# Kernel tuning notes

Measured on AMD Instinct MI355X. Metric: run time of the kernel, lower is better.

## Reference

```python
import jax, jax.numpy as jnp
import numpy as np

B, S, E, H, V = 64, 400, 512, 512, 32000


def setup_inputs() -> dict:
    key = jax.random.key(0)
    ks = jax.random.split(key, 16)
    sc = lambda fan: 1.0 / np.sqrt(fan)
    u = lambda k, shape, fan: jax.random.uniform(k, shape, jnp.float32, -sc(fan), sc(fan))
    mask = jax.random.randint(ks[3], (B, S), 0, 2).astype(bool)
    mask = mask.at[:, 0].set(True)  # ensure at least one valid position per row
    return {
        "decoder_input": jax.random.normal(ks[0], (B, E), jnp.float32),
        "previous_hidden_state": jax.random.normal(ks[1], (B, H), jnp.float32),
        "encoder_output": jax.random.normal(ks[2], (B, S, 2 * H), jnp.float32),
        "mask": mask,
        # GRUCell params (torch layout: weight_ih [3H,E], weight_hh [3H,H])
        "w_ih": u(ks[4], (3 * H, E), H),
        "w_hh": u(ks[5], (3 * H, H), H),
        "b_ih": u(ks[6], (3 * H,), H),
        "b_hh": u(ks[7], (3 * H,), H),
        # Attention params
        "Wh_w": u(ks[8], (H, 2 * H), 2 * H),
        "Wh_b": u(ks[9], (H,), 2 * H),
        "Ws_w": u(ks[10], (H, H), H),
        "Ws_b": u(ks[11], (H,), H),
        "vatt_w": u(ks[12], (1, H), H),  # Linear(H,1,bias=False)
        # Output projections
        "V_w": u(ks[13], (H, 3 * H), 3 * H),
        "V_b": u(ks[13], (H,), 3 * H),
        "Vhat_w": u(ks[14], (V, H), H),
        "Vhat_b": u(ks[15], (V,), H),
    }


def reference(decoder_input, previous_hidden_state, encoder_output, mask,
              w_ih, w_hh, b_ih, b_hh, Wh_w, Wh_b, Ws_w, Ws_b, vatt_w,
              V_w, V_b, Vhat_w, Vhat_b):
    # --- GRUCell step (torch semantics) ---
    gi = decoder_input @ w_ih.T + b_ih                  # [B, 3H]
    gh = previous_hidden_state @ w_hh.T + b_hh          # [B, 3H]
    i_r, i_z, i_n = jnp.split(gi, 3, axis=-1)
    h_r, h_z, h_n = jnp.split(gh, 3, axis=-1)
    r = jax.nn.sigmoid(i_r + h_r)
    z = jax.nn.sigmoid(i_z + h_z)
    n = jnp.tanh(i_n + r * h_n)
    hidden = (1.0 - z) * n + z * previous_hidden_state  # [B, H]

    # --- Additive (Bahdanau) attention ---
    feat = jnp.tanh(encoder_output @ Wh_w.T + Wh_b
                    + (hidden @ Ws_w.T + Ws_b)[:, None, :])   # [B, S, H]
    scores = jnp.einsum('bsh,h->bs', feat, vatt_w[0])          # [B, S]
    scores = jnp.where(mask, scores, -jnp.inf)
    attn_dist = jax.nn.softmax(scores, axis=-1)                # [B, S]

    # --- Context + output projection ---
    context_vector = jnp.einsum('bs,bsd->bd', attn_dist, encoder_output)  # [B, 2H]
    out = jnp.concatenate([hidden, context_vector], axis=-1) @ V_w.T + V_b  # [B, H]
    logits = out @ Vhat_w.T + Vhat_b                                        # [B, V]
    vocab_dist = jax.nn.softmax(logits, axis=-1)
    return (vocab_dist, attn_dist, context_vector, hidden)
```

## Files before the change

### kernel.cpp

```cpp
#include <hip/hip_runtime.h>
#include <hip/hip_bf16.h>
#include <stdint.h>

#define DI __device__ __forceinline__

using f32x4 = __attribute__((ext_vector_type(4))) float;
using s16x8 = __attribute__((ext_vector_type(8))) short;

#define BB 64
#define SS 400
#define HH 512
#define VVOC 32000
#define MTOT (BB*SS)

DI short bf16r(float f){
  __hip_bfloat16 h = __float2bfloat16(f);
  union { __hip_bfloat16 h; short s; } u; u.h = h; return u.s;
}
DI float sigm(float x){ return 1.f/(1.f + __expf(-x)); }
DI float tanhfast(float x){ x = fminf(x, 12.f); float e = __expf(2.f*x); return (e-1.f)/(e+1.f); }

DI void gload16b(const __hip_bfloat16* g, short* l){
  __builtin_amdgcn_global_load_lds(
      (const __attribute__((address_space(1))) __hip_bfloat16*)g,
      (__attribute__((address_space(3))) short*)l, 16, 0, 0);
}

DI float blkmax(float v, float* red, int t){
  #pragma unroll
  for (int o = 32; o; o >>= 1) v = fmaxf(v, __shfl_xor(v, o));
  if ((t & 63) == 0) red[t >> 6] = v;
  __syncthreads();
  v = fmaxf(fmaxf(red[0], red[1]), fmaxf(red[2], red[3]));
  __syncthreads();
  return v;
}
DI float blksum(float v, float* red, int t){
  #pragma unroll
  for (int o = 32; o; o >>= 1) v += __shfl_xor(v, o);
  if ((t & 63) == 0) red[t >> 6] = v;
  __syncthreads();
  v = red[0] + red[1] + red[2] + red[3];
  __syncthreads();
  return v;
}

DI s16x8 cvt8v(f32x4 a, f32x4 b){
  s16x8 o;
  o[0]=bf16r(a[0]); o[1]=bf16r(a[1]); o[2]=bf16r(a[2]); o[3]=bf16r(a[3]);
  o[4]=bf16r(b[0]); o[5]=bf16r(b[1]); o[6]=bf16r(b[2]); o[7]=bf16r(b[3]);
  return o;
}
DI s16x8 cvt8(const float* src){
  return cvt8v(((const f32x4*)src)[0], ((const f32x4*)src)[1]);
}

DI s16x8 fragload16(const short* tile, int rbase, int kk, int l){
  int r = rbase + (l & 15);
  int c = (kk >> 3) + (l >> 4);
  int slot = c ^ (r & 7);
  return *(const s16x8*)(tile + r*64 + slot*8);
}

DI void mfma_small_body(const float* __restrict__ A, const float* __restrict__ W,
                        float* __restrict__ P, int K, int N, int c0, int kseg,
                        short* lsa, short* lsb, int t)
{
  const int kbeg = kseg*64;
  const int l = t & 63, w = t >> 6;
  #pragma unroll
  for (int q = 0; q < 2; ++q) {
    int it = q*256 + t;
    int r = it >> 3, c = it & 7;
    int slot = (c ^ (r & 7)) << 3;
    *(s16x8*)(lsa + r*64 + slot) = cvt8(A + (size_t)r*K + kbeg + c*8);
    *(s16x8*)(lsb + r*64 + slot) = cvt8(W + (size_t)(c0 + r)*K + kbeg + c*8);
  }
  __syncthreads();
  f32x4 acc[4];
  #pragma unroll
  for (int m = 0; m < 4; ++m) { f32x4 z = {0.f,0.f,0.f,0.f}; acc[m] = z; }
  #pragma unroll
  for (int kk = 0; kk < 64; kk += 32) {
    s16x8 bf = fragload16(lsb, w*16, kk, l);
    #pragma unroll
    for (int m = 0; m < 4; ++m) {
      s16x8 af = fragload16(lsa, m*16, kk, l);
      acc[m] = __builtin_amdgcn_mfma_f32_16x16x32_bf16(af, bf, acc[m], 0, 0, 0);
    }
  }
  const int kq = l >> 4, lc = l & 15;
  const int col = c0 + w*16 + lc;
  size_t pbase = (size_t)kseg * 64 * N;
  #pragma unroll
  for (int m = 0; m < 4; ++m)
    #pragma unroll
    for (int j = 0; j < 4; ++j)
      P[pbase + (size_t)(m*16 + kq*4 + j)*N + col] = acc[m][j];
}

__global__ __launch_bounds__(256) void k_pre(
    const float* __restrict__ enc, const float* __restrict__ wh,
    short* __restrict__ enc16, short* __restrict__ wh16,
    const unsigned int* __restrict__ mask, int mwords, int* __restrict__ flags,
    const float* __restrict__ x, const float* __restrict__ hprev,
    const float* __restrict__ w_ih, const float* __restrict__ w_hh,
    float* __restrict__ GI, float* __restrict__ GH)
{
  __shared__ __align__(16) short ls[2][64*64];
  int b = blockIdx.x, t = threadIdx.x;
  if (b < 1600) {
    int i = b*256 + t;
    #pragma unroll
    for (int k = 0; k < 8; ++k) {
      int idx = i + k*409600;
      ((s16x8*)enc16)[idx] = cvt8(enc + (size_t)idx*8);
    }
  } else if (b < 1856) {
    int i = (b-1600)*256 + t;
    ((s16x8*)wh16)[i] = cvt8(wh + (size_t)i*8);
  } else if (b < 1864) {
    __shared__ int f;
    if (t == 0) f = 0;
    __syncthreads();
    int loc = 0;
    for (int i = (b-1856)*256 + t; i < mwords; i += 8*256) loc |= (mask[i] > 1u) ? 1 : 0;
    if (loc) atomicOr(&f, 1);
    __syncthreads();
    if (t == 0) flags[b-1856] = f;
  } else {
    int gb = b - 1864;
    int colI = gb % 24;
    int kseg = (gb / 24) % 8;
    int z    = gb / 192;
    mfma_small_body(z ? hprev : x, z ? w_hh : w_ih, z ? GH : GI,
                    512, 1536, colI*64, kseg, ls[0], ls[1], t);
  }
}

__global__ __launch_bounds__(256) void fused_hidq(
    const float* __restrict__ GI, const float* __restrict__ GH,
    const float* __restrict__ b_ih, const float* __restrict__ b_hh,
    const float* __restrict__ hprev, const float* __restrict__ Ws_w,
    const float* __restrict__ Ws_b, const float* __restrict__ Wh_b,
    float* __restrict__ hid, float* __restrict__ concat, float* __restrict__ Q)
{
  __shared__ float sh[512];
  int b = blockIdx.x, t = threadIdx.x;
  for (int h = t; h < 512; h += 256) {
    float ir=0, iz=0, inn=0, hr=0, hz=0, hn=0;
    #pragma unroll
    for (int s = 0; s < 8; ++s) {
      const float* gi = GI + (size_t)s*(64*1536) + b*1536;
      const float* gh = GH + (size_t)s*(64*1536) + b*1536;
      ir += gi[h];      iz += gi[512+h];  inn += gi[1024+h];
      hr += gh[h];      hz += gh[512+h];  hn  += gh[1024+h];
    }
    ir += b_ih[h]; iz += b_ih[512+h]; inn += b_ih[1024+h];
    hr += b_hh[h]; hz += b_hh[512+h]; hn  += b_hh[1024+h];
    float r = sigm(ir + hr), z = sigm(iz + hz);
    float n = tanhfast(inn + r*hn);
    float hv = (1.f - z)*n + z*hprev[b*512 + h];
    hid[b*512 + h] = hv;
    concat[b*1536 + h] = hv;
    sh[h] = hv;
  }
  __syncthreads();
  for (int c = t; c < 512; c += 256) {
    const f32x4* wrow = (const f32x4*)(Ws_w + (size_t)c*512);
    float a0=0.f, a1=0.f, a2=0.f, a3=0.f;
    #pragma unroll 8
    for (int k4 = 0; k4 < 128; ++k4) {
      f32x4 wv = wrow[k4];
      f32x4 hv = *(const f32x4*)(sh + k4*4);
      a0 += wv[0]*hv[0]; a1 += wv[1]*hv[1]; a2 += wv[2]*hv[2]; a3 += wv[3]*hv[3];
    }
    Q[b*512 + c] = (a0+a1)+(a2+a3) + Ws_b[c] + Wh_b[c];
  }
}

__global__ __launch_bounds__(512) void score_gemm_bf16(
    const __hip_bfloat16* __restrict__ A, const __hip_bfloat16* __restrict__ Bw,
    const float* __restrict__ qv, const float* __restrict__ vb, float* __restrict__ dst)
{
  __shared__ __align__(16) short lsa[128*64];
  __shared__ __align__(16) short lsb[256*64];
  const int t = threadIdx.x;
  const int l = t & 63;
  const int w = t >> 6;
  const int wm = w >> 2;
  const int wn = w & 3;
  const int phys = blockIdx.x;
  const int logical = (phys & 7)*50 + (phys >> 3);
  const int mrow = (logical >> 1) * 128;
  const int colb = logical & 1;
  const int ncol = colb * 256;

  f32x4 acc[4][4];
  #pragma unroll
  for (int m = 0; m < 4; ++m)
    #pragma unroll
    for (int n = 0; n < 4; ++n) { f32x4 z = {0.f,0.f,0.f,0.f}; acc[m][n] = z; }

  for (int k0 = 0; k0 < 1024; k0 += 64) {
    #pragma unroll
    for (int i = 0; i < 2; ++i) {
      int ci = i*512 + t;
      int r = ci >> 3, slot = ci & 7;
      int c = slot ^ (r & 7);
      gload16b(A + (size_t)(mrow + r)*1024 + k0 + c*8, lsa + ci*8);
    }
    #pragma unroll
    for (int i = 0; i < 4; ++i) {
      int ci = i*512 + t;
      int r = ci >> 3, slot = ci & 7;
      int c = slot ^ (r & 7);
      gload16b(Bw + (size_t)(ncol + r)*1024 + k0 + c*8, lsb + ci*8);
    }
    __syncthreads();
    #pragma unroll
    for (int kk = 0; kk < 64; kk += 32) {
      s16x8 bf[4];
      #pragma unroll
      for (int n = 0; n < 4; ++n) bf[n] = fragload16(lsb, wn*64 + n*16, kk, l);
      #pragma unroll
      for (int m = 0; m < 4; ++m) {
        s16x8 af = fragload16(lsa, wm*64 + m*16, kk, l);
        #pragma unroll
        for (int n = 0; n < 4; ++n)
          acc[m][n] = __builtin_amdgcn_mfma_f32_16x16x32_bf16(af, bf[n], acc[m][n], 0, 0, 0);
      }
    }
    __syncthreads();
  }

  const int kq = l >> 4, lc = l & 15;
  float vv[4];
  #pragma unroll
  for (int n = 0; n < 4; ++n) vv[n] = vb[ncol + wn*64 + n*16 + lc];
  const int seg = colb*4 + wn;
  #pragma unroll
  for (int m = 0; m < 4; ++m) {
    #pragma unroll
    for (int j = 0; j < 4; ++j) {
      int r = mrow + wm*64 + m*16 + kq*4 + j;
      int b = r / SS;
      const float* qb = qv + b*HH + ncol + wn*64 + lc;
      float ps = 0.f;
      #pragma unroll
      for (int n = 0; n < 4; ++n) ps += vv[n]*tanhfast(acc[m][n][j] + qb[n*16]);
      #pragma unroll
      for (int o = 1; o < 16; o <<= 1) ps += __shfl_xor(ps, o);
      if (lc == 0) dst[seg*MTOT + r] = ps;
    }
  }
}

__global__ __launch_bounds__(256) void vocab_gemm(
    const float* __restrict__ OUTm, const float* __restrict__ Vhat,
    const float* __restrict__ Vb, float* __restrict__ logits,
    float* __restrict__ MAXP, float* __restrict__ SUMP)
{
  __shared__ __align__(16) short lsa[64*64];
  __shared__ __align__(16) short lsb[64*64];
  __shared__ float red[64][8];
  const int t = threadIdx.x, l = t & 63, w = t >> 6;
  const int vrow0 = blockIdx.x * 64;

  f32x4 acc[4];
  #pragma unroll
  for (int m = 0; m < 4; ++m) { f32x4 z = {0.f,0.f,0.f,0.f}; acc[m] = z; }

  f32x4 pa0[2][2], pb0[2][2], pa1[2][2], pb1[2][2];

  #define VLOAD(pa, pb, k0)                                                     \
    _Pragma("unroll")                                                           \
    for (int q = 0; q < 2; ++q) {                                               \
      int it = q*256 + t; int r = it >> 3, c = it & 7;                          \
      const f32x4* ap = (const f32x4*)(OUTm + (size_t)r*512 + (k0) + c*8);      \
      pa[q][0] = ap[0]; pa[q][1] = ap[1];                                       \
      const f32x4* bp = (const f32x4*)(Vhat + (size_t)(vrow0 + r)*512 + (k0) + c*8); \
      pb[q][0] = bp[0]; pb[q][1] = bp[1];                                       \
    }
  #define VSTEP(pa, pb)                                                         \
    _Pragma("unroll")                                                           \
    for (int q = 0; q < 2; ++q) {                                               \
      int it = q*256 + t; int r = it >> 3, c = it & 7;                          \
      int slot = (c ^ (r & 7)) << 3;                                            \
      *(s16x8*)(lsa + r*64 + slot) = cvt8v(pa[q][0], pa[q][1]);                 \
      *(s16x8*)(lsb + r*64 + slot) = cvt8v(pb[q][0], pb[q][1]);                 \
    }                                                                           \
    __syncthreads();                                                            \
    _Pragma("unroll")                                                           \
    for (int kk = 0; kk < 64; kk += 32) {                                       \
      s16x8 bf = fragload16(lsb, w*16, kk, l);                                  \
      _Pragma("unroll")                                                         \
      for (int m = 0; m < 4; ++m) {                                             \
        s16x8 af = fragload16(lsa, m*16, kk, l);                                \
        acc[m] = __builtin_amdgcn_mfma_f32_16x16x32_bf16(af, bf, acc[m], 0,0,0);\
      }                                                                         \
    }                                                                           \
    __syncthreads();

  VLOAD(pa0, pb0, 0)
  #pragma unroll
  for (int s2 = 0; s2 < 4; ++s2) {
    int k0 = s2*128;
    if (k0 + 64 < 512) { VLOAD(pa1, pb1, k0 + 64) }
    VSTEP(pa0, pb0)
    if (k0 + 128 < 512) { VLOAD(pa0, pb0, k0 + 128) }
    VSTEP(pa1, pb1)
  }
  #undef VLOAD
  #undef VSTEP

  const int kq = l >> 4, lc = l & 15;
  const int voc = vrow0 + w*16 + lc;
  const float bias = Vb[voc];
  #pragma unroll
  for (int m = 0; m < 4; ++m)
    #pragma unroll
    for (int j = 0; j < 4; ++j) {
      acc[m][j] += bias;
      logits[(size_t)(m*16 + kq*4 + j)*VVOC + voc] = acc[m][j];
    }
  #pragma unroll
  for (int m = 0; m < 4; ++m)
    #pragma unroll
    for (int j = 0; j < 4; ++j) {
      float v = acc[m][j];
      #pragma unroll
      for (int o = 1; o < 16; o <<= 1) v = fmaxf(v, __shfl_xor(v, o));
      if (lc == 0) red[m*16 + kq*4 + j][w] = v;
    }
  __syncthreads();
  float gmax[4][4];
  #pragma unroll
  for (int m = 0; m < 4; ++m)
    #pragma unroll
    for (int j = 0; j < 4; ++j) {
      int row = m*16 + kq*4 + j;
      gmax[m][j] = fmaxf(fmaxf(red[row][0], red[row][1]), fmaxf(red[row][2], red[row][3]));
    }
  __syncthreads();
  #pragma unroll
  for (int m = 0; m < 4; ++m)
    #pragma unroll
    for (int j = 0; j < 4; ++j) {
      float s = __expf(acc[m][j] - gmax[m][j]);
      #pragma unroll
      for (int o = 1; o < 16; o <<= 1) s += __shfl_xor(s, o);
      if (lc == 0) red[m*16 + kq*4 + j][4 + w] = s;
    }
  __syncthreads();
  if (t < 64) {
    float M = fmaxf(fmaxf(red[t][0], red[t][1]), fmaxf(red[t][2], red[t][3]));
    float S = red[t][4] + red[t][5] + red[t][6] + red[t][7];
    MAXP[blockIdx.x*64 + t] = M;
    SUMP[blockIdx.x*64 + t] = S;
  }
}

__global__ __launch_bounds__(256) void vnorm(
    const float* __restrict__ MAXP, const float* __restrict__ SUMP,
    float* __restrict__ logits)
{
  __shared__ float red[4];
  int b = blockIdx.x, q = blockIdx.y, t = threadIdx.x;
  float m = -INFINITY;
  for (int i = t; i < 500; i += 256) m = fmaxf(m, MAXP[i*64 + b]);
  m = blkmax(m, red, t);
  float z = 0.f;
  for (int i = t; i < 500; i += 256) z += SUMP[i*64 + b] * __expf(MAXP[i*64 + b] - m);
  z = blksum(z, red, t);
  float inv = 1.f / z;
  f32x4* p = (f32x4*)(logits + (size_t)b*VVOC + q*8000);
  for (int i = t; i < 2000; i += 256) {
    f32x4 v = p[i];
    #pragma unroll
    for (int c = 0; c < 4; ++c) v[c] = __expf(v[c] - m) * inv;
    p[i] = v;
  }
}

__global__ __launch_bounds__(256) void mfma_small(
    const float* __restrict__ A, const float* __restrict__ W,
    float* __restrict__ P, int K, int N)
{
  __shared__ __align__(16) short ls[2][64*64];
  mfma_small_body(A, W, P, K, N, blockIdx.x*64, blockIdx.y, ls[0], ls[1], threadIdx.x);
}

__global__ void combineN(const float* __restrict__ P, const float* __restrict__ b1,
                         float* __restrict__ dstv, int N, int total, int nseg)
{
  int i = blockIdx.x*256 + threadIdx.x;
  if (i >= total) return;
  float a = 0.f;
  for (int s = 0; s < nseg; ++s) a += P[(size_t)s*total + i];
  if (b1) a += b1[i % N];
  dstv[i] = a;
}

__global__ void softmax_s(const float* __restrict__ part, const void* __restrict__ mask,
                          const int* __restrict__ flags, float* __restrict__ attn)
{
  __shared__ float red[4];
  int b = blockIdx.x, t = threadIdx.x;
  bool isbyte = (flags[0]|flags[1]|flags[2]|flags[3]|flags[4]|flags[5]|flags[6]|flags[7]) != 0;
  float sc0, sc1 = -INFINITY;
  {
    float v = 0.f;
    #pragma unroll
    for (int p = 0; p < 8; ++p) v += part[p*MTOT + b*SS + t];
    bool mv = isbyte ? (((const unsigned char*)mask)[b*SS + t] != 0)
                     : (((const int*)mask)[b*SS + t] != 0);
    sc0 = mv ? v : -INFINITY;
  }
  int s1 = t + 256;
  if (s1 < SS) {
    float v = 0.f;
    #pragma unroll
    for (int p = 0; p < 8; ++p) v += part[p*MTOT + b*SS + s1];
    bool mv = isbyte ? (((const unsigned char*)mask)[b*SS + s1] != 0)
                     : (((const int*)mask)[b*SS + s1] != 0);
    sc1 = mv ? v : -INFINITY;
  }
  float mx = blkmax(fmaxf(sc0, sc1), red, t);
  float e0 = __expf(sc0 - mx), e1 = __expf(sc1 - mx);
  float sum = blksum(e0 + e1, red, t);
  float inv = 1.f / sum;
  attn[b*SS + t] = e0 * inv;
  if (s1 < SS) attn[b*SS + s1] = e1 * inv;
}

__global__ void ctx_part(const float* __restrict__ attn, const unsigned int* __restrict__ enc16,
                         float* __restrict__ CTXP)
{
  int b = blockIdx.x, dh = blockIdx.y, sq = blockIdx.z;
  int d0 = dh*512 + threadIdx.x*2;
  const float* a = attn + b*SS + sq*50;
  const unsigned int* e = enc16 + (((size_t)(b*SS + sq*50)*1024 + d0) >> 1);
  float lo = 0.f, hi = 0.f;
  #pragma unroll 5
  for (int s = 0; s < 50; ++s) {
    unsigned int u = e[(size_t)s*512];
    float av = a[s];
    lo += av * __uint_as_float(u << 16);
    hi += av * __uint_as_float(u & 0xffff0000u);
  }
  float* dst = CTXP + (size_t)sq*65536 + b*1024 + d0;
  dst[0] = lo; dst[1] = hi;
}

__global__ void ctx_combine(const float* __restrict__ CTXP, float* __restrict__ ctx,
                            float* __restrict__ concat)
{
  int b = blockIdx.x;
  for (int d = threadIdx.x; d < 1024; d += 256) {
    float s = 0.f;
    #pragma unroll
    for (int q = 0; q < 8; ++q) s += CTXP[q*65536 + b*1024 + d];
    ctx[b*1024 + d] = s;
    concat[b*1536 + 512 + d] = s;
  }
}

extern "C" void kernel_launch(void* const* d_in, const int* in_sizes, int n_in,
                              void* d_out, int out_size, void* d_ws, size_t ws_size,
                              hipStream_t stream) {
  (void)in_sizes; (void)n_in; (void)out_size; (void)ws_size;
  const float* x      = (const float*)d_in[0];
  const float* hprev  = (const float*)d_in[1];
  const float* enc    = (const float*)d_in[2];
  const void*  mask   = d_in[3];
  const float* w_ih   = (const float*)d_in[4];
  const float* w_hh   = (const float*)d_in[5];
  const float* b_ih   = (const float*)d_in[6];
  const float* b_hh   = (const float*)d_in[7];
  const float* Wh_w   = (const float*)d_in[8];
  const float* Wh_b   = (const float*)d_in[9];
  const float* Ws_w   = (const float*)d_in[10];
  const float* Ws_b   = (const float*)d_in[11];
  const float* vatt   = (const float*)d_in[12];
  const float* V_w    = (const float*)d_in[13];
  const float* V_b    = (const float*)d_in[14];
  const float* Vhat_w = (const float*)d_in[15];
  const float* Vhat_b = (const float*)d_in[16];

  float* out   = (float*)d_out;
  float* vocab = out;
  float* attn  = out + 2048000;
  float* ctx   = out + 2073600;
  float* hid   = out + 2139136;

  float* WS     = (float*)d_ws;
  int*   FLAGS  = (int*)d_ws;
  float* GI     = WS + 16;
  float* GH     = GI + 786432;
  float* Q      = GH + 786432;
  float* OUT    = Q + 32768;
  float* PART   = OUT + 32768;
  float* MAXP   = PART + 204800;
  float* SUMP   = MAXP + 32000;
  float* CTXP   = SUMP + 32000;
  float* OUTP   = CTXP + 524288;
  float* CONCAT = OUTP + 786432;
  float* ENDF   = CONCAT + 98304;
  size_t f32_bytes = ((size_t)((char*)ENDF - (char*)d_ws) + 15) & ~(size_t)15;
  short* ENC16 = (short*)((char*)d_ws + f32_bytes);
  short* WH16  = ENC16 + (size_t)25600*1024;

  k_pre<<<dim3(2248), 256, 0, stream>>>(enc, Wh_w, ENC16, WH16,
                                        (const unsigned int*)mask, 6400, FLAGS,
                                        x, hprev, w_ih, w_hh, GI, GH);
  fused_hidq<<<dim3(64), 256, 0, stream>>>(GI, GH, b_ih, b_hh, hprev,
                                           Ws_w, Ws_b, Wh_b, hid, CONCAT, Q);
  score_gemm_bf16<<<dim3(400), 512, 0, stream>>>(
      (const __hip_bfloat16*)ENC16, (const __hip_bfloat16*)WH16, Q, vatt, PART);
  softmax_s<<<dim3(64), 256, 0, stream>>>(PART, mask, FLAGS, attn);
  ctx_part<<<dim3(64, 2, 8), 256, 0, stream>>>(attn, (const unsigned int*)ENC16, CTXP);
  ctx_combine<<<dim3(64), 256, 0, stream>>>(CTXP, ctx, CONCAT);
  mfma_small<<<dim3(8, 24), 256, 0, stream>>>(CONCAT, V_w, OUTP, 1536, 512);
  combineN<<<dim3(128), 256, 0, stream>>>(OUTP, V_b, OUT, 512, 32768, 24);
  vocab_gemm<<<dim3(500), 256, 0, stream>>>(OUT, Vhat_w, Vhat_b, vocab, MAXP, SUMP);
  vnorm<<<dim3(64, 4), 256, 0, stream>>>(MAXP, SUMP, vocab);
}
```

Baseline: 160.6 us.

## Convert encoder to bf16 inside score GEMM; drop separate encoder conversion pass

The separate pass that wrote a bf16 copy of the 105 MB fp32 encoder output is removed. The score GEMM now loads fp32 encoder tiles into registers, converts them to bf16 and writes them to LDS, double-buffered against the MFMA loop, using a smaller 64x128 tile and 1600 blocks. ctx_part now reads the fp32 encoder directly. The GRU gate and the Ws projection are split into separate kernels, with the projection run on the MFMA split-K path. This avoids writing and re-reading a bf16 copy of the encoder, at the cost of twice the read bytes in ctx_part and more launches.

```diff
diff --git a/kernel.cpp b/kernel.cpp
--- a/kernel.cpp
+++ b/kernel.cpp
@@ -4,6 +4,7 @@
 
 #define DI __device__ __forceinline__
 
+using f32x2 = __attribute__((ext_vector_type(2))) float;
 using f32x4 = __attribute__((ext_vector_type(4))) float;
 using s16x8 = __attribute__((ext_vector_type(8))) short;
 
@@ -100,8 +101,7 @@
 }
 
 __global__ __launch_bounds__(256) void k_pre(
-    const float* __restrict__ enc, const float* __restrict__ wh,
-    short* __restrict__ enc16, short* __restrict__ wh16,
+    const float* __restrict__ wh, short* __restrict__ wh16,
     const unsigned int* __restrict__ mask, int mwords, int* __restrict__ flags,
     const float* __restrict__ x, const float* __restrict__ hprev,
     const float* __restrict__ w_ih, const float* __restrict__ w_hh,
@@ -109,27 +109,20 @@
 {
   __shared__ __align__(16) short ls[2][64*64];
   int b = blockIdx.x, t = threadIdx.x;
-  if (b < 1600) {
+  if (b < 256) {
     int i = b*256 + t;
-    #pragma unroll
-    for (int k = 0; k < 8; ++k) {
-      int idx = i + k*409600;
-      ((s16x8*)enc16)[idx] = cvt8(enc + (size_t)idx*8);
-    }
-  } else if (b < 1856) {
-    int i = (b-1600)*256 + t;
     ((s16x8*)wh16)[i] = cvt8(wh + (size_t)i*8);
-  } else if (b < 1864) {
+  } else if (b < 264) {
     __shared__ int f;
     if (t == 0) f = 0;
     __syncthreads();
     int loc = 0;
-    for (int i = (b-1856)*256 + t; i < mwords; i += 8*256) loc |= (mask[i] > 1u) ? 1 : 0;
+    for (int i = (b-256)*256 + t; i < mwords; i += 8*256) loc |= (mask[i] > 1u) ? 1 : 0;
     if (loc) atomicOr(&f, 1);
     __syncthreads();
-    if (t == 0) flags[b-1856] = f;
+    if (t == 0) flags[b-256] = f;
   } else {
-    int gb = b - 1864;
+    int gb = b - 264;
     int colI = gb % 24;
     int kseg = (gb / 24) % 8;
     int z    = gb / 192;
@@ -138,112 +131,137 @@
   }
 }
 
-__global__ __launch_bounds__(256) void fused_hidq(
-    const float* __restrict__ GI, const float* __restrict__ GH,
-    const float* __restrict__ b_ih, const float* __restrict__ b_hh,
-    const float* __restrict__ hprev, const float* __restrict__ Ws_w,
-    const float* __restrict__ Ws_b, const float* __restrict__ Wh_b,
-    float* __restrict__ hid, float* __restrict__ concat, float* __restrict__ Q)
-{
-  __shared__ float sh[512];
-  int b = blockIdx.x, t = threadIdx.x;
-  for (int h = t; h < 512; h += 256) {
-    float ir=0, iz=0, inn=0, hr=0, hz=0, hn=0;
-    #pragma unroll
-    for (int s = 0; s < 8; ++s) {
-      const float* gi = GI + (size_t)s*(64*1536) + b*1536;
-      const float* gh = GH + (size_t)s*(64*1536) + b*1536;
-      ir += gi[h];      iz += gi[512+h];  inn += gi[1024+h];
-      hr += gh[h];      hz += gh[512+h];  hn  += gh[1024+h];
-    }
-    ir += b_ih[h]; iz += b_ih[512+h]; inn += b_ih[1024+h];
-    hr += b_hh[h]; hz += b_hh[512+h]; hn  += b_hh[1024+h];
-    float r = sigm(ir + hr), z = sigm(iz + hz);
-    float n = tanhfast(inn + r*hn);
-    float hv = (1.f - z)*n + z*hprev[b*512 + h];
-    hid[b*512 + h] = hv;
-    concat[b*1536 + h] = hv;
-    sh[h] = hv;
-  }
-  __syncthreads();
-  for (int c = t; c < 512; c += 256) {
-    const f32x4* wrow = (const f32x4*)(Ws_w + (size_t)c*512);
-    float a0=0.f, a1=0.f, a2=0.f, a3=0.f;
-    #pragma unroll 8
-    for (int k4 = 0; k4 < 128; ++k4) {
-      f32x4 wv = wrow[k4];
-      f32x4 hv = *(const f32x4*)(sh + k4*4);
-      a0 += wv[0]*hv[0]; a1 += wv[1]*hv[1]; a2 += wv[2]*hv[2]; a3 += wv[3]*hv[3];
-    }
-    Q[b*512 + c] = (a0+a1)+(a2+a3) + Ws_b[c] + Wh_b[c];
-  }
-}
-
-__global__ __launch_bounds__(512) void score_gemm_bf16(
-    const __hip_bfloat16* __restrict__ A, const __hip_bfloat16* __restrict__ Bw,
+__global__ void gru_gate(const float* __restrict__ GI, const float* __restrict__ GH,
+                         const float* __restrict__ b_ih, const float* __restrict__ b_hh,
+                         const float* __restrict__ hprev, float* __restrict__ hid,
+                         float* __restrict__ concat)
+{
+  int i = blockIdx.x*256 + threadIdx.x;
+  int b = i >> 9, h = i & 511;
+  float ir=0, iz=0, inn=0, hr=0, hz=0, hn=0;
+  #pragma unroll
+  for (int s = 0; s < 8; ++s) {
+    const float* gi = GI + (size_t)s*(64*1536) + b*1536;
+    const float* gh = GH + (size_t)s*(64*1536) + b*1536;
+    ir += gi[h];      iz += gi[512+h];  inn += gi[1024+h];
+    hr += gh[h];      hz += gh[512+h];  hn  += gh[1024+h];
+  }
+  ir += b_ih[h]; iz += b_ih[512+h]; inn += b_ih[1024+h];
+  hr += b_hh[h]; hz += b_hh[512+h]; hn  += b_hh[1024+h];
+  float r = sigm(ir + hr), z = sigm(iz + hz);
+  float n = tanhfast(inn + r*hn);
+  float hv = (1.f - z)*n + z*hprev[i];
+  hid[i] = hv;
+  concat[b*1536 + h] = hv;
+}
+
+__global__ __launch_bounds__(256) void mfma_small(
+    const float* __restrict__ A, const float* __restrict__ W,
+    float* __restrict__ P, int K, int N)
+{
+  __shared__ __align__(16) short ls[2][64*64];
+  mfma_small_body(A, W, P, K, N, blockIdx.x*64, blockIdx.y, ls[0], ls[1], threadIdx.x);
+}
+
+__global__ void combineN(const float* __restrict__ P, const float* __restrict__ b1,
+                         const float* __restrict__ b2, float* __restrict__ dstv,
+                         int N, int total, int nseg)
+{
+  int i = blockIdx.x*256 + threadIdx.x;
+  if (i >= total) return;
+  float a = 0.f;
+  for (int s = 0; s < nseg; ++s) a += P[(size_t)s*total + i];
+  int c = i % N;
+  if (b1) a += b1[c];
+  if (b2) a += b2[c];
+  dstv[i] = a;
+}
+
+__global__ __launch_bounds__(256) void score_gemm_bf16(
+    const float* __restrict__ A, const __hip_bfloat16* __restrict__ Bw,
     const float* __restrict__ qv, const float* __restrict__ vb, float* __restrict__ dst)
 {
-  __shared__ __align__(16) short lsa[128*64];
-  __shared__ __align__(16) short lsb[256*64];
+  __shared__ __align__(16) short lsa[2][64*64];
+  __shared__ __align__(16) short lsb[2][128*64];
   const int t = threadIdx.x;
   const int l = t & 63;
   const int w = t >> 6;
-  const int wm = w >> 2;
-  const int wn = w & 3;
+  const int wm = w >> 1;
+  const int wn = w & 1;
   const int phys = blockIdx.x;
-  const int logical = (phys & 7)*50 + (phys >> 3);
-  const int mrow = (logical >> 1) * 128;
-  const int colb = logical & 1;
-  const int ncol = colb * 256;
-
-  f32x4 acc[4][4];
-  #pragma unroll
-  for (int m = 0; m < 4; ++m)
+  const int logical = (phys & 7)*200 + (phys >> 3);
+  const int mrow = (logical >> 2) * 64;
+  const int colb = logical & 3;
+  const int ncol = colb * 128;
+
+  const int ar = t >> 2;
+  const int aq = t & 3;
+  const float* abase = A + (size_t)(mrow + ar)*1024 + aq*16;
+  const int as0 = ((2*aq    ) ^ (ar & 7)) << 3;
+  const int as1 = ((2*aq + 1) ^ (ar & 7)) << 3;
+
+  f32x4 acc[2][4];
+  #pragma unroll
+  for (int m = 0; m < 2; ++m)
     #pragma unroll
     for (int n = 0; n < 4; ++n) { f32x4 z = {0.f,0.f,0.f,0.f}; acc[m][n] = z; }
 
-  for (int k0 = 0; k0 < 1024; k0 += 64) {
-    #pragma unroll
-    for (int i = 0; i < 2; ++i) {
-      int ci = i*512 + t;
-      int r = ci >> 3, slot = ci & 7;
-      int c = slot ^ (r & 7);
-      gload16b(A + (size_t)(mrow + r)*1024 + k0 + c*8, lsa + ci*8);
-    }
-    #pragma unroll
-    for (int i = 0; i < 4; ++i) {
-      int ci = i*512 + t;
-      int r = ci >> 3, slot = ci & 7;
-      int c = slot ^ (r & 7);
-      gload16b(Bw + (size_t)(ncol + r)*1024 + k0 + c*8, lsb + ci*8);
-    }
-    __syncthreads();
+  f32x4 pa0, pa1, pa2, pa3;
+  #define A_LOAD(k0) { const f32x4* ap = (const f32x4*)(abase + (k0));            \
+                       pa0 = ap[0]; pa1 = ap[1]; pa2 = ap[2]; pa3 = ap[3]; }
+  #define A_WRITE(buf) { *(s16x8*)(&lsa[buf][ar*64] + as0) = cvt8v(pa0, pa1);     \
+                         *(s16x8*)(&lsa[buf][ar*64] + as1) = cvt8v(pa2, pa3); }
+  #define B_STAGE(buf, k0)                                                        \
+    _Pragma("unroll")                                                              \
+    for (int i = 0; i < 4; ++i) {                                                  \
+      int ci = i*256 + t;                                                          \
+      int r = ci >> 3, slot = ci & 7;                                              \
+      int c = slot ^ (r & 7);                                                      \
+      gload16b(Bw + (size_t)(ncol + r)*1024 + (k0) + c*8, &lsb[buf][ci*8]);        \
+    }
+
+  A_LOAD(0)
+  B_STAGE(0, 0)
+  A_WRITE(0)
+  __syncthreads();
+
+  int cur = 0;
+  for (int k = 0; k < 16; ++k) {
+    if (k < 15) {
+      A_LOAD((k+1)*64)
+      B_STAGE(cur ^ 1, (k+1)*64)
+    }
     #pragma unroll
     for (int kk = 0; kk < 64; kk += 32) {
       s16x8 bf[4];
       #pragma unroll
-      for (int n = 0; n < 4; ++n) bf[n] = fragload16(lsb, wn*64 + n*16, kk, l);
+      for (int n = 0; n < 4; ++n) bf[n] = fragload16(lsb[cur], wn*64 + n*16, kk, l);
       #pragma unroll
-      for (int m = 0; m < 4; ++m) {
-        s16x8 af = fragload16(lsa, wm*64 + m*16, kk, l);
+      for (int m = 0; m < 2; ++m) {
+        s16x8 af = fragload16(lsa[cur], wm*32 + m*16, kk, l);
         #pragma unroll
         for (int n = 0; n < 4; ++n)
           acc[m][n] = __builtin_amdgcn_mfma_f32_16x16x32_bf16(af, bf[n], acc[m][n], 0, 0, 0);
       }
     }
+    if (k < 15) A_WRITE(cur ^ 1)
     __syncthreads();
-  }
+    cur ^= 1;
+  }
+  #undef A_LOAD
+  #undef A_WRITE
+  #undef B_STAGE
 
   const int kq = l >> 4, lc = l & 15;
   float vv[4];
   #pragma unroll
   for (int n = 0; n < 4; ++n) vv[n] = vb[ncol + wn*64 + n*16 + lc];
-  const int seg = colb*4 + wn;
-  #pragma unroll
-  for (int m = 0; m < 4; ++m) {
+  const int seg = colb*2 + wn;
+  #pragma unroll
+  for (int m = 0; m < 2; ++m) {
     #pragma unroll
     for (int j = 0; j < 4; ++j) {
-      int r = mrow + wm*64 + m*16 + kq*4 + j;
+      int r = mrow + wm*32 + m*16 + kq*4 + j;
       int b = r / SS;
       const float* qb = qv + b*HH + ncol + wn*64 + lc;
       float ps = 0.f;
@@ -383,25 +401,6 @@
   }
 }
 
-__global__ __launch_bounds__(256) void mfma_small(
-    const float* __restrict__ A, const float* __restrict__ W,
-    float* __restrict__ P, int K, int N)
-{
-  __shared__ __align__(16) short ls[2][64*64];
-  mfma_small_body(A, W, P, K, N, blockIdx.x*64, blockIdx.y, ls[0], ls[1], threadIdx.x);
-}
-
-__global__ void combineN(const float* __restrict__ P, const float* __restrict__ b1,
-                         float* __restrict__ dstv, int N, int total, int nseg)
-{
-  int i = blockIdx.x*256 + threadIdx.x;
-  if (i >= total) return;
-  float a = 0.f;
-  for (int s = 0; s < nseg; ++s) a += P[(size_t)s*total + i];
-  if (b1) a += b1[i % N];
-  dstv[i] = a;
-}
-
 __global__ void softmax_s(const float* __restrict__ part, const void* __restrict__ mask,
                           const int* __restrict__ flags, float* __restrict__ attn)
 {
@@ -434,20 +433,20 @@
   if (s1 < SS) attn[b*SS + s1] = e1 * inv;
 }
 
-__global__ void ctx_part(const float* __restrict__ attn, const unsigned int* __restrict__ enc16,
+__global__ void ctx_part(const float* __restrict__ attn, const float* __restrict__ enc,
                          float* __restrict__ CTXP)
 {
   int b = blockIdx.x, dh = blockIdx.y, sq = blockIdx.z;
   int d0 = dh*512 + threadIdx.x*2;
   const float* a = attn + b*SS + sq*50;
-  const unsigned int* e = enc16 + (((size_t)(b*SS + sq*50)*1024 + d0) >> 1);
+  const float* e = enc + (size_t)(b*SS + sq*50)*1024 + d0;
   float lo = 0.f, hi = 0.f;
   #pragma unroll 5
   for (int s = 0; s < 50; ++s) {
-    unsigned int u = e[(size_t)s*512];
+    f32x2 u = *(const f32x2*)(e + (size_t)s*1024);
     float av = a[s];
-    lo += av * __uint_as_float(u << 16);
-    hi += av * __uint_as_float(u & 0xffff0000u);
+    lo += av * u[0];
+    hi += av * u[1];
   }
   float* dst = CTXP + (size_t)sq*65536 + b*1024 + d0;
   dst[0] = lo; dst[1] = hi;
@@ -498,7 +497,8 @@
   int*   FLAGS  = (int*)d_ws;
   float* GI     = WS + 16;
   float* GH     = GI + 786432;
-  float* Q      = GH + 786432;
+  float* QP     = GH + 786432;
+  float* Q      = QP + 262144;
   float* OUT    = Q + 32768;
   float* PART   = OUT + 32768;
   float* MAXP   = PART + 204800;
@@ -508,21 +508,20 @@
   float* CONCAT = OUTP + 786432;
   float* ENDF   = CONCAT + 98304;
   size_t f32_bytes = ((size_t)((char*)ENDF - (char*)d_ws) + 15) & ~(size_t)15;
-  short* ENC16 = (short*)((char*)d_ws + f32_bytes);
-  short* WH16  = ENC16 + (size_t)25600*1024;
-
-  k_pre<<<dim3(2248), 256, 0, stream>>>(enc, Wh_w, ENC16, WH16,
-                                        (const unsigned int*)mask, 6400, FLAGS,
-                                        x, hprev, w_ih, w_hh, GI, GH);
-  fused_hidq<<<dim3(64), 256, 0, stream>>>(GI, GH, b_ih, b_hh, hprev,
-                                           Ws_w, Ws_b, Wh_b, hid, CONCAT, Q);
-  score_gemm_bf16<<<dim3(400), 512, 0, stream>>>(
-      (const __hip_bfloat16*)ENC16, (const __hip_bfloat16*)WH16, Q, vatt, PART);
+  short* WH16  = (short*)((char*)d_ws + f32_bytes);
+
+  k_pre<<<dim3(648), 256, 0, stream>>>(Wh_w, WH16, (const unsigned int*)mask, 6400, FLAGS,
+                                       x, hprev, w_ih, w_hh, GI, GH);
+  gru_gate<<<dim3(128), 256, 0, stream>>>(GI, GH, b_ih, b_hh, hprev, hid, CONCAT);
+  mfma_small<<<dim3(8, 8), 256, 0, stream>>>(hid, Ws_w, QP, 512, 512);
+  combineN<<<dim3(128), 256, 0, stream>>>(QP, Ws_b, Wh_b, Q, 512, 32768, 8);
+  score_gemm_bf16<<<dim3(1600), 256, 0, stream>>>(
+      enc, (const __hip_bfloat16*)WH16, Q, vatt, PART);
   softmax_s<<<dim3(64), 256, 0, stream>>>(PART, mask, FLAGS, attn);
-  ctx_part<<<dim3(64, 2, 8), 256, 0, stream>>>(attn, (const unsigned int*)ENC16, CTXP);
+  ctx_part<<<dim3(64, 2, 8), 256, 0, stream>>>(attn, enc, CTXP);
   ctx_combine<<<dim3(64), 256, 0, stream>>>(CTXP, ctx, CONCAT);
   mfma_small<<<dim3(8, 24), 256, 0, stream>>>(CONCAT, V_w, OUTP, 1536, 512);
-  combineN<<<dim3(128), 256, 0, stream>>>(OUTP, V_b, OUT, 512, 32768, 24);
+  combineN<<<dim3(128), 256, 0, stream>>>(OUTP, V_b, nullptr, OUT, 512, 32768, 24);
   vocab_gemm<<<dim3(500), 256, 0, stream>>>(OUT, Vhat_w, Vhat_b, vocab, MAXP, SUMP);
   vnorm<<<dim3(64, 4), 256, 0, stream>>>(MAXP, SUMP, vocab);
 }
```

Measured after the change: 152.6 us. -5.0%, faster.
